# Kernel tuning notes

Hardware: AMD Instinct MI355X
Metric: run time of the kernel (lower is better)

## Reference

```python
import jax, jax.numpy as jnp
import numpy as np

E = 256        # HP.EMBED_SIZE
R = 8          # number of derivation rules / MLPs
S = 512        # number of sequential derivation steps
N = 256        # nodes produced per step
N_INIT = 1024  # initial axiom (thax) embeddings
TOTAL = N_INIT + S * N  # 132096 rows in the vectors buffer
M = 65536      # masked nodes fed to eval_net


def setup_inputs() -> dict:
    key = jax.random.key(0)
    ks = jax.random.split(key, 12)
    rng = np.random.default_rng(0)

    init_vecs = jax.random.normal(ks[0], (N_INIT, E), jnp.float32)
    # rule MLPs: concat(2 parents) -> E (relu) -> E
    W1 = jax.random.normal(ks[1], (R, 2 * E, E), jnp.float32) * (1.0 / np.sqrt(2 * E))
    b1 = jnp.zeros((R, E), jnp.float32)
    W2 = jax.random.normal(ks[2], (R, E, E), jnp.float32) * (1.0 / np.sqrt(E))
    b2 = jnp.zeros((R, E), jnp.float32)
    # eval net: E -> E (relu) -> 1
    eval_W1 = jax.random.normal(ks[3], (E, E), jnp.float32) * (1.0 / np.sqrt(E))
    eval_b1 = jnp.zeros((E,), jnp.float32)
    eval_W2 = jax.random.normal(ks[4], (E, 1), jnp.float32) * (1.0 / np.sqrt(E))
    eval_b2 = jnp.zeros((1,), jnp.float32)

    # step s writes rows [N_INIT + s*N, N_INIT + (s+1)*N)
    ind_steps = (N_INIT + np.arange(S * N, dtype=np.int32)).reshape(S, N)
    # parents drawn causally from already-computed prefix [0, N_INIT + s*N)
    highs = (N_INIT + np.arange(S, dtype=np.int64) * N)[:, None, None]
    pars_ind_steps = (rng.random((S, N, 2)) * highs).astype(np.int32)
    rule_steps = rng.integers(0, R, size=(S,)).astype(np.int32)
    mask = rng.integers(0, TOTAL, size=(M,)).astype(np.int32)

    pos = jax.random.uniform(ks[5], (M,), jnp.float32)
    neg = jax.random.uniform(ks[6], (M,), jnp.float32)
    target = jnp.round(jax.random.uniform(ks[7], (M,), jnp.float32))

    return {
        'init_vecs': init_vecs, 'W1': W1, 'b1': b1, 'W2': W2, 'b2': b2,
        'eval_W1': eval_W1, 'eval_b1': eval_b1, 'eval_W2': eval_W2, 'eval_b2': eval_b2,
        'pos': pos, 'neg': neg, 'target': target,
        'ind_steps': jnp.asarray(ind_steps), 'pars_ind_steps': jnp.asarray(pars_ind_steps),
        'rule_steps': jnp.asarray(rule_steps), 'mask': jnp.asarray(mask),
    }


def reference(init_vecs, W1, b1, W2, b2, eval_W1, eval_b1, eval_W2, eval_b2,
              pos, neg, target, ind_steps, pars_ind_steps, rule_steps, mask):
    vectors = jnp.zeros((TOTAL, E), init_vecs.dtype).at[:N_INIT].set(init_vecs)

    def step(vec, xs):
        inds, pars, r = xs            # [N], [N,2], scalar rule id
        p = vec[pars].reshape(N, 2 * E)   # gather parents
        h = jax.nn.relu(p @ W1[r] + b1[r])
        out = h @ W2[r] + b2[r]
        return vec.at[inds].set(out), None  # scatter new node embeddings

    vectors, _ = jax.lax.scan(step, vectors, (ind_steps, pars_ind_steps, rule_steps))

    x = vectors[mask]
    val = (jax.nn.relu(x @ eval_W1 + eval_b1) @ eval_W2 + eval_b2)[:, 0]

    # pos_weight = POS_WEIGHT_EXTRA * tot_neg / tot_pos (constant w.r.t. grads)
    pw = jax.lax.stop_gradient(jnp.sum(neg) / jnp.maximum(jnp.sum(pos), 1.0))
    # BCEWithLogitsLoss(pos_weight, reduction='none')
    contrib = pw * target * jax.nn.softplus(-val) + (1.0 - target) * jax.nn.softplus(val)
    loss = jnp.sum((pos + neg) * contrib)
    posOK = jnp.sum(pos * (val >= 0))
    negOK = jnp.sum(neg * (val < 0))
    return loss, posOK, negOK
```

## Files before the change

### kernel.cpp

```cpp
#include <hip/hip_runtime.h>
#include <math.h>

#define EMB   256
#define TWOE  512
#define NINIT 1024
#define NSTEP 512
#define NPS   256
#define TOTAL (NINIT + NSTEP * NPS)
#define MM    65536
#define NNODE (NSTEP * NPS)
#define NKEY  2048
#define BTH   512
#define TROWS 32

typedef short s16x8 __attribute__((ext_vector_type(8)));
typedef float f32x4 __attribute__((ext_vector_type(4)));

#define OFF_VECH  0ull
#define OFF_VECL  ((size_t)TOTAL * EMB * 2)
#define OFF_VAL   (2ull * (size_t)TOTAL * EMB * 2)
#define OFF_CNT   (OFF_VAL + (size_t)MM * 4)
#define OFF_ACC   (OFF_CNT + 4096)
#define OFF_PW    (OFF_ACC + 64)
#define OFF_KCNT  (OFF_PW + 192)
#define OFF_KOFS  (OFF_KCNT + (size_t)NKEY * 4)
#define OFF_NL    (OFF_KOFS + (size_t)NKEY * 4)
#define OFF_BROWS (OFF_NL + 256)


__device__ __forceinline__ void store_dev_u32(unsigned* p, unsigned v) {
  asm volatile("global_store_dword %0, %1, off sc0 sc1" :: "v"(p), "v"(v) : "memory");
}
__device__ __forceinline__ void store_dev_b64(void* p, uint2 v) {
  asm volatile("global_store_dwordx2 %0, %1, off sc0 sc1" :: "v"(p), "v"(v) : "memory");
}
__device__ __forceinline__ void store_dev_b128(void* p, uint4 v) {
  store_dev_b64(p, make_uint2(v.x, v.y));
  store_dev_b64((char*)p + 8, make_uint2(v.z, v.w));
}
__device__ __forceinline__ unsigned load_dev_u32(const unsigned* p) {
  unsigned r;
  asm volatile("global_load_dword %0, %1, off sc0 sc1\n\ts_waitcnt vmcnt(0)"
               : "=v"(r) : "v"(p) : "memory");
  return r;
}

__device__ __forceinline__ void gbar_full(unsigned* gc, unsigned* gep) {
  asm volatile("s_waitcnt vmcnt(0)" ::: "memory");
  __syncthreads();
  if (threadIdx.x == 0) {
    unsigned old = __hip_atomic_fetch_add(gc, 1u, __ATOMIC_RELAXED, __HIP_MEMORY_SCOPE_AGENT);
    unsigned tgt = old / 256u + 1u;
    if ((old & 255u) == 255u) store_dev_u32(gep, tgt);
    else while (load_dev_u32(gep) < tgt) __builtin_amdgcn_s_sleep(1);
  }
  __syncthreads();
}

__device__ __forceinline__ void split8(const float* f, uint4& h4, uint4& l4) {
  unsigned hu[8], lu[8];
  #pragma unroll
  for (int i = 0; i < 8; ++i) {
    unsigned u = __builtin_bit_cast(unsigned, f[i]);
    float rh = __builtin_bit_cast(float, u & 0xffff0000u);
    float rl = f[i] - rh;
    hu[i] = u >> 16;
    lu[i] = __builtin_bit_cast(unsigned, rl) >> 16;
  }
  h4 = make_uint4(hu[0] | (hu[1] << 16), hu[2] | (hu[3] << 16),
                  hu[4] | (hu[5] << 16), hu[6] | (hu[7] << 16));
  l4 = make_uint4(lu[0] | (lu[1] << 16), lu[2] | (lu[3] << 16),
                  lu[4] | (lu[5] << 16), lu[6] | (lu[7] << 16));
}

__global__ void zero_scratch(unsigned* cnt, double* acc) {
  for (int i = threadIdx.x; i < 1024; i += 256) cnt[i] = 0u;
  if (threadIdx.x < 8) acc[threadIdx.x] = 0.0;
}

__global__ void init_convert(const float* __restrict__ src,
                             unsigned short* __restrict__ vh,
                             unsigned short* __restrict__ vl) {
  int slot = blockIdx.x * blockDim.x + threadIdx.x;
  float f[8];
  *(float4*)&f[0] = reinterpret_cast<const float4*>(src)[slot * 2];
  *(float4*)&f[4] = reinterpret_cast<const float4*>(src)[slot * 2 + 1];
  uint4 h4, l4;
  split8(f, h4, l4);
  *(uint4*)(vh + (size_t)slot * 8) = h4;
  *(uint4*)(vl + (size_t)slot * 8) = l4;
}

__global__ __launch_bounds__(1024)
void prepass(const int* __restrict__ pars, const int* __restrict__ rules,
             int* __restrict__ kcnt, int* __restrict__ kofs,
             int* __restrict__ brows, int* __restrict__ nlp)
{
  __shared__ unsigned char slvl[TOTAL];
  __shared__ int scnt[NKEY];
  __shared__ int sofs[NKEY];
  __shared__ int swmax[16];
  const int t = threadIdx.x;
  for (int i = t; i < NINIT; i += 1024) slvl[i] = 0;
  for (int k = t; k < NKEY; k += 1024) scnt[k] = 0;
  __syncthreads();
  int lmax = 0;
  for (int s = 0; s < NSTEP; ++s) {
    if (t < NPS) {
      int i = s * NPS + t;
      int l1 = slvl[pars[2 * i]];
      int l2 = slvl[pars[2 * i + 1]];
      int lv = 1 + (l1 > l2 ? l1 : l2);
      slvl[NINIT + i] = (unsigned char)lv;
      if (lv > lmax) lmax = lv;
    }
    __syncthreads();
  }
  for (int o = 32; o; o >>= 1) lmax = max(lmax, __shfl_down(lmax, o));
  if ((t & 63) == 0) swmax[t >> 6] = lmax;
  __syncthreads();
  if (t == 0) {
    int m = 0;
    for (int w = 0; w < 16; ++w) m = max(m, swmax[w]);
    nlp[0] = m;
  }
  for (int i = t; i < NNODE; i += 1024) {
    int key = (int)slvl[NINIT + i] * 8 + rules[i >> 8];
    atomicAdd(&scnt[key], 1);
  }
  __syncthreads();
  if (t == 0) {
    int run = 0;
    for (int k = 0; k < NKEY; ++k) {
      kofs[k] = run; sofs[k] = run; kcnt[k] = scnt[k]; run += scnt[k];
    }
  }
  __syncthreads();
  for (int i = t; i < NNODE; i += 1024) {
    int key = (int)slvl[NINIT + i] * 8 + rules[i >> 8];
    int pos = atomicAdd(&sofs[key], 1);
    brows[pos] = i;
  }
}

__global__ __launch_bounds__(BTH, 1)
void scan_kernel(const float* __restrict__ W1, const float* __restrict__ b1,
                 const float* __restrict__ W2, const float* __restrict__ b2,
                 const int* __restrict__ pars,
                 unsigned short* __restrict__ vech, unsigned short* __restrict__ vecl,
                 const int* __restrict__ kcnt, const int* __restrict__ kofs,
                 const int* __restrict__ brows, const int* __restrict__ nlp,
                 unsigned* __restrict__ cnt)
{
  __shared__ short sW[2][2][8192];
  __shared__ float hL[TROWS][260];
  __shared__ int spar[2 * TROWS];
  __shared__ int sorow[TROWS];
  const int tid = threadIdx.x;
  const int bid = blockIdx.x;
  const int lane = tid & 63;
  const int w = tid >> 6;
  const int rw = w & 1, cw = w >> 1;
  const int row16 = lane & 15, kb8 = (lane >> 4) << 3;
  const int arow = (rw << 4) + row16;
  unsigned* gc  = cnt;
  unsigned* gep = cnt + 32;
  const int NL = nlp[0];
  const int xcd = bid & 7, jb = bid >> 3;

  const int g0 = tid >> 6, l0 = tid & 63;
  const int g1 = g0 + 8,   l1 = l0;

  for (int lv = 1; lv <= NL; ++lv) {
    int cum[9]; cum[0] = 0;
    int cnts[8], ofss[8];
    #pragma unroll
    for (int r = 0; r < 8; ++r) {
      int c = kcnt[lv * 8 + r];
      cnts[r] = c; ofss[r] = kofs[lv * 8 + r];
      cum[r + 1] = cum[r] + ((c + TROWS - 1) >> 5);
    }
    const int G = cum[8];
    const int q = G >> 3, rm = G & 7;
    const int Gx = q + (xcd < rm ? 1 : 0);
    const int sx = xcd * q + (xcd < rm ? xcd : rm);
    for (int j = jb; j < Gx; j += 32) {
      const int g = sx + j;
      int rr = 0;
      while (g >= cum[rr + 1]) ++rr;
      const int t0 = g - cum[rr];
      const int cnt_b = cnts[rr], ofs_b = ofss[rr];
      const int tbase = t0 * TROWS;
      const float* __restrict__ W1r = W1 + (size_t)rr * TWOE * EMB;
      const float* __restrict__ W2r = W2 + (size_t)rr * EMB * EMB;

      __syncthreads();
      if (tid < 2 * TROWS) {
        int slot = tbase + (tid >> 1);
        if (slot >= cnt_b) slot = cnt_b - 1;
        int node = brows[ofs_b + slot];
        spar[tid] = pars[2 * node + (tid & 1)];
        if ((tid & 1) == 0) sorow[tid >> 1] = NINIT + node;
      }
      float f[16];
      {
        const float* p0 = W1r + (size_t)((l0 >> 4) << 3) * EMB + (g0 << 4) + (l0 & 15);
        const float* p1 = W1r + (size_t)((l1 >> 4) << 3) * EMB + (g1 << 4) + (l1 & 15);
        #pragma unroll
        for (int i = 0; i < 8; ++i) { f[i] = p0[i * EMB]; f[8 + i] = p1[i * EMB]; }
        uint4 h4, l4;
        split8(f, h4, l4);
        *(uint4*)&sW[0][0][tid * 8] = h4;
        *(uint4*)&sW[0][1][tid * 8] = l4;
        split8(f + 8, h4, l4);
        *(uint4*)&sW[0][0][(tid + 512) * 8] = h4;
        *(uint4*)&sW[0][1][(tid + 512) * 8] = l4;
      }
      __syncthreads();
      const int par0 = spar[2 * arow], par1 = spar[2 * arow + 1];
      float b1v[4];
      #pragma unroll
      for (int g4 = 0; g4 < 4; ++g4)
        b1v[g4] = b1[rr * EMB + (cw << 6) + (g4 << 4) + row16];

      uint4 ahA, alA;
      {
        size_t off = (size_t)par0 * EMB + kb8;
        ahA = *(const uint4*)(vech + off);
        alA = *(const uint4*)(vecl + off);
      }
      f32x4 acc[4] = {{0,0,0,0},{0,0,0,0},{0,0,0,0},{0,0,0,0}};
      int curb = 0;
      for (int c = 0; c < 16; ++c) {
        const float* nsrc = (c < 15) ? W1r : W2r;
        const int nkb = (c < 15) ? (c + 1) * 32 : 0;
        {
          const float* p0 = nsrc + (size_t)(nkb + ((l0 >> 4) << 3)) * EMB + (g0 << 4) + (l0 & 15);
          const float* p1 = nsrc + (size_t)(nkb + ((l1 >> 4) << 3)) * EMB + (g1 << 4) + (l1 & 15);
          #pragma unroll
          for (int i = 0; i < 8; ++i) { f[i] = p0[i * EMB]; f[8 + i] = p1[i * EMB]; }
        }
        uint4 ahB = ahA, alB = alA;
        if (c < 15) {
          int kglob = (c + 1) * 32 + kb8;
          int par = (kglob >> 8) ? par1 : par0;
          size_t off = (size_t)par * EMB + (kglob & 255);
          ahB = *(const uint4*)(vech + off);
          alB = *(const uint4*)(vecl + off);
        }
        {
          s16x8 Ah = __builtin_bit_cast(s16x8, ahA);
          s16x8 Al = __builtin_bit_cast(s16x8, alA);
          const s16x8* bph = (const s16x8*)&sW[curb][0][0];
          const s16x8* bpl = (const s16x8*)&sW[curb][1][0];
          #pragma unroll
          for (int g4 = 0; g4 < 4; ++g4) {
            int gi = ((cw << 2) + g4) * 64 + lane;
            s16x8 Bh = bph[gi], Bl = bpl[gi];
            acc[g4] = __builtin_amdgcn_mfma_f32_16x16x32_bf16(Ah, Bh, acc[g4], 0, 0, 0);
            acc[g4] = __builtin_amdgcn_mfma_f32_16x16x32_bf16(Ah, Bl, acc[g4], 0, 0, 0);
            acc[g4] = __builtin_amdgcn_mfma_f32_16x16x32_bf16(Al, Bh, acc[g4], 0, 0, 0);
          }
        }
        {
          uint4 h4, l4;
          split8(f, h4, l4);
          *(uint4*)&sW[curb ^ 1][0][tid * 8] = h4;
          *(uint4*)&sW[curb ^ 1][1][tid * 8] = l4;
          split8(f + 8, h4, l4);
          *(uint4*)&sW[curb ^ 1][0][(tid + 512) * 8] = h4;
          *(uint4*)&sW[curb ^ 1][1][(tid + 512) * 8] = l4;
        }
        __syncthreads();
        curb ^= 1;
        ahA = ahB; alA = alB;
      }
      #pragma unroll
      for (int g4 = 0; g4 < 4; ++g4) {
        #pragma unroll
        for (int jj = 0; jj < 4; ++jj)
          hL[(rw << 4) + ((lane >> 4) << 2) + jj][(cw << 6) + (g4 << 4) + row16] =
              fmaxf(acc[g4][jj] + b1v[g4], 0.f);
      }
      __syncthreads();
      float b2v[4];
      #pragma unroll
      for (int g4 = 0; g4 < 4; ++g4)
        b2v[g4] = b2[rr * EMB + (cw << 6) + (g4 << 4) + row16];
      f32x4 acc2[4] = {{0,0,0,0},{0,0,0,0},{0,0,0,0},{0,0,0,0}};
      for (int c2 = 0; c2 < 8; ++c2) {
        if (c2 < 7) {
          const int nkb = (c2 + 1) * 32;
          const float* p0 = W2r + (size_t)(nkb + ((l0 >> 4) << 3)) * EMB + (g0 << 4) + (l0 & 15);
          const float* p1 = W2r + (size_t)(nkb + ((l1 >> 4) << 3)) * EMB + (g1 << 4) + (l1 & 15);
          #pragma unroll
          for (int i = 0; i < 8; ++i) { f[i] = p0[i * EMB]; f[8 + i] = p1[i * EMB]; }
        }
        uint4 a2h4, a2l4;
        {
          int kb = c2 * 32 + kb8;
          float af[8];
          *(float4*)&af[0] = *(const float4*)&hL[arow][kb];
          *(float4*)&af[4] = *(const float4*)&hL[arow][kb + 4];
          split8(af, a2h4, a2l4);
        }
        {
          s16x8 Ah = __builtin_bit_cast(s16x8, a2h4);
          s16x8 Al = __builtin_bit_cast(s16x8, a2l4);
          const s16x8* bph = (const s16x8*)&sW[curb][0][0];
          const s16x8* bpl = (const s16x8*)&sW[curb][1][0];
          #pragma unroll
          for (int g4 = 0; g4 < 4; ++g4) {
            int gi = ((cw << 2) + g4) * 64 + lane;
            s16x8 Bh = bph[gi], Bl = bpl[gi];
            acc2[g4] = __builtin_amdgcn_mfma_f32_16x16x32_bf16(Ah, Bh, acc2[g4], 0, 0, 0);
            acc2[g4] = __builtin_amdgcn_mfma_f32_16x16x32_bf16(Ah, Bl, acc2[g4], 0, 0, 0);
            acc2[g4] = __builtin_amdgcn_mfma_f32_16x16x32_bf16(Al, Bh, acc2[g4], 0, 0, 0);
          }
        }
        if (c2 < 7) {
          uint4 h4, l4;
          split8(f, h4, l4);
          *(uint4*)&sW[curb ^ 1][0][tid * 8] = h4;
          *(uint4*)&sW[curb ^ 1][1][tid * 8] = l4;
          split8(f + 8, h4, l4);
          *(uint4*)&sW[curb ^ 1][0][(tid + 512) * 8] = h4;
          *(uint4*)&sW[curb ^ 1][1][(tid + 512) * 8] = l4;
          __syncthreads();
          curb ^= 1;
        }
      }
      __syncthreads();
      #pragma unroll
      for (int g4 = 0; g4 < 4; ++g4) {
        #pragma unroll
        for (int jj = 0; jj < 4; ++jj)
          hL[(rw << 4) + ((lane >> 4) << 2) + jj][(cw << 6) + (g4 << 4) + row16] =
              acc2[g4][jj] + b2v[g4];
      }
      __syncthreads();
      #pragma unroll
      for (int u = 0; u < 2; ++u) {
        int s = tid + u * 512;
        int row = s >> 5, c8 = (s & 31) * 8;
        float of[8];
        *(float4*)&of[0] = *(const float4*)&hL[row][c8];
        *(float4*)&of[4] = *(const float4*)&hL[row][c8 + 4];
        uint4 h4, l4;
        split8(of, h4, l4);
        if (tbase + row < cnt_b) {
          size_t off = (size_t)sorow[row] * EMB + c8;
          store_dev_b128(vech + off, h4);
          store_dev_b128(vecl + off, l4);
        }
      }
    }
    gbar_full(gc, gep);
  }
}

__global__ void reduce_pn(const float* __restrict__ pos, const float* __restrict__ neg,
                          double* acc) {
  double sp = 0.0, sn = 0.0;
  for (int m = blockIdx.x * blockDim.x + threadIdx.x; m < MM; m += gridDim.x * blockDim.x) {
    sp += (double)pos[m]; sn += (double)neg[m];
  }
  for (int o = 32; o; o >>= 1) { sp += __shfl_down(sp, o); sn += __shfl_down(sn, o); }
  __shared__ double rp[4], rn[4];
  int wid = threadIdx.x >> 6, lane = threadIdx.x & 63;
  if (lane == 0) { rp[wid] = sp; rn[wid] = sn; }
  __syncthreads();
  if (threadIdx.x == 0) {
    double tp = 0.0, tn = 0.0;
    for (int w = 0; w < 4; ++w) { tp += rp[w]; tn += rn[w]; }
    atomicAdd(&acc[0], tp); atomicAdd(&acc[1], tn);
  }
}

__global__ void pw_kernel(const double* __restrict__ acc, float* __restrict__ pw) {
  pw[0] = (float)(acc[1] / fmax(acc[0], 1.0));
}

__global__ __launch_bounds__(256)
void eval_kernel(const unsigned short* __restrict__ vh, const unsigned short* __restrict__ vl,
                 const int* __restrict__ mask,
                 const float* __restrict__ eW1, const float* __restrict__ eb1,
                 const float* __restrict__ eW2, const float* __restrict__ eb2,
                 float* __restrict__ val)
{
  __shared__ float xL[64][36];
  __shared__ float wLx[32][260];
  __shared__ int mrow[64];
  const int tid = threadIdx.x;
  const int a = tid >> 4, b = tid & 15;
  const int m0 = blockIdx.x * 64;
  if (tid < 64) mrow[tid] = mask[m0 + tid];
  __syncthreads();

  float acc[4][16];
  #pragma unroll
  for (int i = 0; i < 4; ++i)
    #pragma unroll
    for (int j = 0; j < 16; ++j) acc[i][j] = 0.f;

  for (int c = 0; c < 8; ++c) {
    const int e0 = c * 32;
    for (int idx = tid; idx < 64 * 4; idx += 256) {
      int rr = idx >> 2, u = idx & 3;
      size_t off = (size_t)mrow[rr] * EMB + e0 + u * 8;
      uint4 hv = *(const uint4*)(vh + off);
      uint4 lv = *(const uint4*)(vl + off);
      const unsigned* hu = (const unsigned*)&hv;
      const unsigned* lu = (const unsigned*)&lv;
      float fo[8];
      #pragma unroll
      for (int jj = 0; jj < 4; ++jj) {
        fo[2 * jj] = __builtin_bit_cast(float, (hu[jj] & 0xffffu) << 16) +
                     __builtin_bit_cast(float, (lu[jj] & 0xffffu) << 16);
        fo[2 * jj + 1] = __builtin_bit_cast(float, hu[jj] & 0xffff0000u) +
                         __builtin_bit_cast(float, lu[jj] & 0xffff0000u);
      }
      *(float4*)&xL[rr][u * 8] = *(float4*)&fo[0];
      *(float4*)&xL[rr][u * 8 + 4] = *(float4*)&fo[4];
    }
    for (int idx = tid; idx < 32 * 64; idx += 256) {
      int e = idx >> 6, k4 = idx & 63;
      reinterpret_cast<float4*>(&wLx[e][0])[k4] =
          reinterpret_cast<const float4*>(eW1 + (size_t)(e0 + e) * EMB)[k4];
    }
    __syncthreads();
    #pragma unroll 4
    for (int e = 0; e < 32; ++e) {
      float xs[4];
      #pragma unroll
      for (int rr = 0; rr < 4; ++rr) xs[rr] = xL[a * 4 + rr][e];
      const float4* wr = reinterpret_cast<const float4*>(&wLx[e][0]) + b * 4;
      float wk[16];
      *reinterpret_cast<float4*>(&wk[0])  = wr[0];
      *reinterpret_cast<float4*>(&wk[4])  = wr[1];
      *reinterpret_cast<float4*>(&wk[8])  = wr[2];
      *reinterpret_cast<float4*>(&wk[12]) = wr[3];
      #pragma unroll
      for (int rr = 0; rr < 4; ++rr)
        #pragma unroll
        for (int kk = 0; kk < 16; ++kk)
          acc[rr][kk] = fmaf(xs[rr], wk[kk], acc[rr][kk]);
    }
    __syncthreads();
  }

  float eb2v = eb2[0];
  float pv[4];
  #pragma unroll
  for (int rr = 0; rr < 4; ++rr) {
    float s = 0.f;
    #pragma unroll
    for (int kk = 0; kk < 16; ++kk) {
      float h = acc[rr][kk] + eb1[b * 16 + kk];
      h = fmaxf(h, 0.f);
      s += h * eW2[b * 16 + kk];
    }
    pv[rr] = s;
  }
  #pragma unroll
  for (int m = 1; m < 16; m <<= 1) {
    #pragma unroll
    for (int rr = 0; rr < 4; ++rr) pv[rr] += __shfl_xor(pv[rr], m);
  }
  if (b == 0) {
    #pragma unroll
    for (int rr = 0; rr < 4; ++rr) val[m0 + a * 4 + rr] = pv[rr] + eb2v;
  }
}

__global__ void loss_kernel(const float* __restrict__ val, const float* __restrict__ pos,
                            const float* __restrict__ neg, const float* __restrict__ tgt,
                            const float* __restrict__ pwp, double* acc)
{
  const float pw = pwp[0];
  double l = 0.0, pk = 0.0, nk = 0.0;
  for (int m = blockIdx.x * blockDim.x + threadIdx.x; m < MM; m += gridDim.x * blockDim.x) {
    float v = val[m], p = pos[m], n = neg[m], t = tgt[m];
    float lp = log1pf(expf(-fabsf(v)));
    float spn = fmaxf(-v, 0.f) + lp;
    float spp = fmaxf(v, 0.f) + lp;
    float contrib = pw * t * spn + (1.f - t) * spp;
    l += (double)((p + n) * contrib);
    if (v >= 0.f) pk += (double)p; else nk += (double)n;
  }
  for (int o = 32; o; o >>= 1) {
    l += __shfl_down(l, o); pk += __shfl_down(pk, o); nk += __shfl_down(nk, o);
  }
  __shared__ double s0[4], s1[4], s2[4];
  int wid = threadIdx.x >> 6, lane = threadIdx.x & 63;
  if (lane == 0) { s0[wid] = l; s1[wid] = pk; s2[wid] = nk; }
  __syncthreads();
  if (threadIdx.x == 0) {
    double ta = 0.0, tb = 0.0, tc = 0.0;
    for (int w = 0; w < 4; ++w) { ta += s0[w]; tb += s1[w]; tc += s2[w]; }
    atomicAdd(&acc[2], ta); atomicAdd(&acc[3], tb); atomicAdd(&acc[4], tc);
  }
}

__global__ void writeout(const double* __restrict__ acc, float* __restrict__ out) {
  if (threadIdx.x == 0) {
    out[0] = (float)acc[2];
    out[1] = (float)acc[3];
    out[2] = (float)acc[4];
  }
}

extern "C" void kernel_launch(void* const* d_in, const int* in_sizes, int n_in,
                              void* d_out, int out_size, void* d_ws, size_t ws_size,
                              hipStream_t stream)
{
  (void)in_sizes; (void)n_in; (void)out_size; (void)ws_size;
  const float* init_vecs = (const float*)d_in[0];
  const float* W1  = (const float*)d_in[1];
  const float* b1  = (const float*)d_in[2];
  const float* W2  = (const float*)d_in[3];
  const float* b2  = (const float*)d_in[4];
  const float* eW1 = (const float*)d_in[5];
  const float* eb1 = (const float*)d_in[6];
  const float* eW2 = (const float*)d_in[7];
  const float* eb2 = (const float*)d_in[8];
  const float* pos = (const float*)d_in[9];
  const float* neg = (const float*)d_in[10];
  const float* tgt = (const float*)d_in[11];
  const int* pars  = (const int*)d_in[13];
  const int* rules = (const int*)d_in[14];
  const int* mask  = (const int*)d_in[15];

  char* ws = (char*)d_ws;
  unsigned short* vech = (unsigned short*)(ws + OFF_VECH);
  unsigned short* vecl = (unsigned short*)(ws + OFF_VECL);
  float*    val   = (float*)(ws + OFF_VAL);
  unsigned* cnt   = (unsigned*)(ws + OFF_CNT);
  double*   acc   = (double*)(ws + OFF_ACC);
  float*    pw    = (float*)(ws + OFF_PW);
  int*      kcnt  = (int*)(ws + OFF_KCNT);
  int*      kofs  = (int*)(ws + OFF_KOFS);
  int*      nlp   = (int*)(ws + OFF_NL);
  int*      brows = (int*)(ws + OFF_BROWS);

  zero_scratch<<<1, 256, 0, stream>>>(cnt, acc);
  prepass<<<1, 1024, 0, stream>>>(pars, rules, kcnt, kofs, brows, nlp);
  init_convert<<<128, 256, 0, stream>>>(init_vecs, vech, vecl);
  scan_kernel<<<256, BTH, 0, stream>>>(W1, b1, W2, b2, pars, vech, vecl,
                                       kcnt, kofs, brows, nlp, cnt);
  reduce_pn<<<128, 256, 0, stream>>>(pos, neg, acc);
  pw_kernel<<<1, 1, 0, stream>>>(acc, pw);
  eval_kernel<<<1024, 256, 0, stream>>>(vech, vecl, mask, eW1, eb1, eW2, eb2, val);
  loss_kernel<<<128, 256, 0, stream>>>(val, pos, neg, tgt, pw, acc);
  writeout<<<1, 1, 0, stream>>>(acc, (float*)d_out);
}
```

Baseline: 1.253 ms.

## Presplit rule weights to bf16 hi/lo once and read MFMA operands from global

Adds a presplit kernel that converts W1/W2 for every rule into a bf16 hi/lo MFMA-ready layout in workspace once per call. The scan kernel then loads B operands straight from global/L2 instead of converting fp32 weights per tile into double-buffered LDS, which removes per-chunk split work and many __syncthreads. The level prepass is also split into its own 256-thread kernel that prefetches parent indices in batches of eight steps, followed by a separate bucketing kernel. The trade-off is that weight reads now depend on L2/global latency with no LDS staging, adding pressure on the memory hierarchy.

```diff
diff --git a/kernel.cpp b/kernel.cpp
--- a/kernel.cpp
+++ b/kernel.cpp
@@ -12,20 +12,24 @@
 #define NKEY  2048
 #define BTH   512
 #define TROWS 32
+#define CHK_SH  16384
+#define RULE_SH (24 * CHK_SH)
 
 typedef short s16x8 __attribute__((ext_vector_type(8)));
 typedef float f32x4 __attribute__((ext_vector_type(4)));
 
-#define OFF_VECH  0ull
-#define OFF_VECL  ((size_t)TOTAL * EMB * 2)
-#define OFF_VAL   (2ull * (size_t)TOTAL * EMB * 2)
-#define OFF_CNT   (OFF_VAL + (size_t)MM * 4)
-#define OFF_ACC   (OFF_CNT + 4096)
-#define OFF_PW    (OFF_ACC + 64)
-#define OFF_KCNT  (OFF_PW + 192)
-#define OFF_KOFS  (OFF_KCNT + (size_t)NKEY * 4)
-#define OFF_NL    (OFF_KOFS + (size_t)NKEY * 4)
-#define OFF_BROWS (OFF_NL + 256)
+#define OFF_VECH   0ull
+#define OFF_VECL   ((size_t)TOTAL * EMB * 2)
+#define OFF_VAL    (2ull * (size_t)TOTAL * EMB * 2)
+#define OFF_CNT    (OFF_VAL + (size_t)MM * 4)
+#define OFF_ACC    (OFF_CNT + 4096)
+#define OFF_PW     (OFF_ACC + 64)
+#define OFF_KCNT   (OFF_PW + 192)
+#define OFF_KOFS   (OFF_KCNT + (size_t)NKEY * 4)
+#define OFF_NL     (OFF_KOFS + (size_t)NKEY * 4)
+#define OFF_BROWS  (OFF_NL + 256)
+#define OFF_LVL8   (OFF_BROWS + (size_t)NNODE * 4)
+#define OFF_WSPLIT (OFF_LVL8 + 132352)
 
 
 __device__ __forceinline__ void store_dev_u32(unsigned* p, unsigned v) {
@@ -91,68 +95,121 @@
   *(uint4*)(vl + (size_t)slot * 8) = l4;
 }
 
+__global__ __launch_bounds__(512)
+void presplit(const float* __restrict__ W1, const float* __restrict__ W2,
+              short* __restrict__ Ws)
+{
+  const int blk = blockIdx.x;
+  const int r = blk / 24, c = blk % 24;
+  const float* src; int kbase;
+  if (c < 16) { src = W1 + (size_t)r * TWOE * EMB; kbase = c * 32; }
+  else        { src = W2 + (size_t)r * EMB * EMB;  kbase = (c - 16) * 32; }
+  short* dst = Ws + (size_t)blk * CHK_SH;
+  const int tid = threadIdx.x;
+  #pragma unroll
+  for (int u = 0; u < 2; ++u) {
+    int qq = tid + u * 512;
+    int g = qq >> 6, l = qq & 63;
+    const float* p = src + (size_t)(kbase + ((l >> 4) << 3)) * EMB + (g << 4) + (l & 15);
+    float f[8];
+    #pragma unroll
+    for (int i = 0; i < 8; ++i) f[i] = p[i * EMB];
+    uint4 h4, l4;
+    split8(f, h4, l4);
+    *(uint4*)(dst + (size_t)qq * 8) = h4;
+    *(uint4*)(dst + 8192 + (size_t)qq * 8) = l4;
+  }
+}
+
+__global__ __launch_bounds__(256)
+void prepass_levels(const int* __restrict__ pars, unsigned char* __restrict__ lvl8,
+                    int* __restrict__ nlp)
+{
+  __shared__ unsigned char slvl[TOTAL];
+  __shared__ int swmax[4];
+  const int t = threadIdx.x;
+  for (int i = t; i < NINIT; i += 256) slvl[i] = 0;
+  __syncthreads();
+  int Pa[8], Pb[8];
+  #pragma unroll
+  for (int w = 0; w < 8; ++w) {
+    Pa[w] = pars[2 * (w * NPS + t)];
+    Pb[w] = pars[2 * (w * NPS + t) + 1];
+  }
+  int lmax = 0;
+  for (int s0 = 0; s0 < NSTEP; s0 += 8) {
+    int Na[8], Nb[8];
+    if (s0 + 8 < NSTEP) {
+      #pragma unroll
+      for (int w = 0; w < 8; ++w) {
+        Na[w] = pars[2 * ((s0 + 8 + w) * NPS + t)];
+        Nb[w] = pars[2 * ((s0 + 8 + w) * NPS + t) + 1];
+      }
+    } else {
+      #pragma unroll
+      for (int w = 0; w < 8; ++w) { Na[w] = 0; Nb[w] = 0; }
+    }
+    #pragma unroll
+    for (int w = 0; w < 8; ++w) {
+      int l1 = slvl[Pa[w]], l2 = slvl[Pb[w]];
+      int lv = 1 + (l1 > l2 ? l1 : l2);
+      slvl[NINIT + (s0 + w) * NPS + t] = (unsigned char)lv;
+      if (lv > lmax) lmax = lv;
+      __syncthreads();
+    }
+    #pragma unroll
+    for (int w = 0; w < 8; ++w) { Pa[w] = Na[w]; Pb[w] = Nb[w]; }
+  }
+  const unsigned* sv = (const unsigned*)slvl;
+  unsigned* gv = (unsigned*)lvl8;
+  for (int i = t; i < TOTAL / 4; i += 256) gv[i] = sv[i];
+  for (int o = 32; o; o >>= 1) lmax = max(lmax, __shfl_down(lmax, o));
+  if ((t & 63) == 0) swmax[t >> 6] = lmax;
+  __syncthreads();
+  if (t == 0) {
+    int m = 0;
+    for (int w = 0; w < 4; ++w) m = max(m, swmax[w]);
+    nlp[0] = m;
+  }
+}
+
 __global__ __launch_bounds__(1024)
-void prepass(const int* __restrict__ pars, const int* __restrict__ rules,
-             int* __restrict__ kcnt, int* __restrict__ kofs,
-             int* __restrict__ brows, int* __restrict__ nlp)
-{
-  __shared__ unsigned char slvl[TOTAL];
+void prepass_bucket(const unsigned char* __restrict__ lvl8, const int* __restrict__ rules,
+                    int* __restrict__ kcnt, int* __restrict__ kofs,
+                    int* __restrict__ brows)
+{
   __shared__ int scnt[NKEY];
   __shared__ int sofs[NKEY];
-  __shared__ int swmax[16];
   const int t = threadIdx.x;
-  for (int i = t; i < NINIT; i += 1024) slvl[i] = 0;
   for (int k = t; k < NKEY; k += 1024) scnt[k] = 0;
   __syncthreads();
-  int lmax = 0;
-  for (int s = 0; s < NSTEP; ++s) {
-    if (t < NPS) {
-      int i = s * NPS + t;
-      int l1 = slvl[pars[2 * i]];
-      int l2 = slvl[pars[2 * i + 1]];
-      int lv = 1 + (l1 > l2 ? l1 : l2);
-      slvl[NINIT + i] = (unsigned char)lv;
-      if (lv > lmax) lmax = lv;
-    }
-    __syncthreads();
-  }
-  for (int o = 32; o; o >>= 1) lmax = max(lmax, __shfl_down(lmax, o));
-  if ((t & 63) == 0) swmax[t >> 6] = lmax;
-  __syncthreads();
-  if (t == 0) {
-    int m = 0;
-    for (int w = 0; w < 16; ++w) m = max(m, swmax[w]);
-    nlp[0] = m;
-  }
   for (int i = t; i < NNODE; i += 1024) {
-    int key = (int)slvl[NINIT + i] * 8 + rules[i >> 8];
+    int key = (int)lvl8[NINIT + i] * 8 + rules[i >> 8];
     atomicAdd(&scnt[key], 1);
   }
   __syncthreads();
   if (t == 0) {
     int run = 0;
     for (int k = 0; k < NKEY; ++k) {
-      kofs[k] = run; sofs[k] = run; kcnt[k] = scnt[k]; run += scnt[k];
+      sofs[k] = run; kofs[k] = run; kcnt[k] = scnt[k]; run += scnt[k];
     }
   }
   __syncthreads();
   for (int i = t; i < NNODE; i += 1024) {
-    int key = (int)slvl[NINIT + i] * 8 + rules[i >> 8];
+    int key = (int)lvl8[NINIT + i] * 8 + rules[i >> 8];
     int pos = atomicAdd(&sofs[key], 1);
     brows[pos] = i;
   }
 }
 
 __global__ __launch_bounds__(BTH, 1)
-void scan_kernel(const float* __restrict__ W1, const float* __restrict__ b1,
-                 const float* __restrict__ W2, const float* __restrict__ b2,
-                 const int* __restrict__ pars,
+void scan_kernel(const short* __restrict__ Ws, const float* __restrict__ b1,
+                 const float* __restrict__ b2, const int* __restrict__ pars,
                  unsigned short* __restrict__ vech, unsigned short* __restrict__ vecl,
                  const int* __restrict__ kcnt, const int* __restrict__ kofs,
                  const int* __restrict__ brows, const int* __restrict__ nlp,
                  unsigned* __restrict__ cnt)
 {
-  __shared__ short sW[2][2][8192];
   __shared__ float hL[TROWS][260];
   __shared__ int spar[2 * TROWS];
   __shared__ int sorow[TROWS];
@@ -160,16 +217,13 @@
   const int bid = blockIdx.x;
   const int lane = tid & 63;
   const int w = tid >> 6;
-  const int rw = w & 1, cw = w >> 1;
+  const int rw = w & 1, cwb = (w >> 1) << 2;
   const int row16 = lane & 15, kb8 = (lane >> 4) << 3;
   const int arow = (rw << 4) + row16;
   unsigned* gc  = cnt;
   unsigned* gep = cnt + 32;
   const int NL = nlp[0];
   const int xcd = bid & 7, jb = bid >> 3;
-
-  const int g0 = tid >> 6, l0 = tid & 63;
-  const int g1 = g0 + 8,   l1 = l0;
 
   for (int lv = 1; lv <= NL; ++lv) {
     int cum[9]; cum[0] = 0;
@@ -191,8 +245,7 @@
       const int t0 = g - cum[rr];
       const int cnt_b = cnts[rr], ofs_b = ofss[rr];
       const int tbase = t0 * TROWS;
-      const float* __restrict__ W1r = W1 + (size_t)rr * TWOE * EMB;
-      const float* __restrict__ W2r = W2 + (size_t)rr * EMB * EMB;
+      const short* __restrict__ Wr = Ws + (size_t)rr * RULE_SH;
 
       __syncthreads();
       if (tid < 2 * TROWS) {
@@ -202,26 +255,12 @@
         spar[tid] = pars[2 * node + (tid & 1)];
         if ((tid & 1) == 0) sorow[tid >> 1] = NINIT + node;
       }
-      float f[16];
-      {
-        const float* p0 = W1r + (size_t)((l0 >> 4) << 3) * EMB + (g0 << 4) + (l0 & 15);
-        const float* p1 = W1r + (size_t)((l1 >> 4) << 3) * EMB + (g1 << 4) + (l1 & 15);
-        #pragma unroll
-        for (int i = 0; i < 8; ++i) { f[i] = p0[i * EMB]; f[8 + i] = p1[i * EMB]; }
-        uint4 h4, l4;
-        split8(f, h4, l4);
-        *(uint4*)&sW[0][0][tid * 8] = h4;
-        *(uint4*)&sW[0][1][tid * 8] = l4;
-        split8(f + 8, h4, l4);
-        *(uint4*)&sW[0][0][(tid + 512) * 8] = h4;
-        *(uint4*)&sW[0][1][(tid + 512) * 8] = l4;
-      }
       __syncthreads();
       const int par0 = spar[2 * arow], par1 = spar[2 * arow + 1];
       float b1v[4];
       #pragma unroll
       for (int g4 = 0; g4 < 4; ++g4)
-        b1v[g4] = b1[rr * EMB + (cw << 6) + (g4 << 4) + row16];
+        b1v[g4] = b1[rr * EMB + ((cwb + g4) << 4) + row16];
 
       uint4 ahA, alA;
       {
@@ -230,16 +269,8 @@
         alA = *(const uint4*)(vecl + off);
       }
       f32x4 acc[4] = {{0,0,0,0},{0,0,0,0},{0,0,0,0},{0,0,0,0}};
-      int curb = 0;
+      #pragma unroll 2
       for (int c = 0; c < 16; ++c) {
-        const float* nsrc = (c < 15) ? W1r : W2r;
-        const int nkb = (c < 15) ? (c + 1) * 32 : 0;
-        {
-          const float* p0 = nsrc + (size_t)(nkb + ((l0 >> 4) << 3)) * EMB + (g0 << 4) + (l0 & 15);
-          const float* p1 = nsrc + (size_t)(nkb + ((l1 >> 4) << 3)) * EMB + (g1 << 4) + (l1 & 15);
-          #pragma unroll
-          for (int i = 0; i < 8; ++i) { f[i] = p0[i * EMB]; f[8 + i] = p1[i * EMB]; }
-        }
         uint4 ahB = ahA, alB = alA;
         if (c < 15) {
           int kglob = (c + 1) * 32 + kb8;
@@ -248,86 +279,52 @@
           ahB = *(const uint4*)(vech + off);
           alB = *(const uint4*)(vecl + off);
         }
-        {
-          s16x8 Ah = __builtin_bit_cast(s16x8, ahA);
-          s16x8 Al = __builtin_bit_cast(s16x8, alA);
-          const s16x8* bph = (const s16x8*)&sW[curb][0][0];
-          const s16x8* bpl = (const s16x8*)&sW[curb][1][0];
-          #pragma unroll
-          for (int g4 = 0; g4 < 4; ++g4) {
-            int gi = ((cw << 2) + g4) * 64 + lane;
-            s16x8 Bh = bph[gi], Bl = bpl[gi];
-            acc[g4] = __builtin_amdgcn_mfma_f32_16x16x32_bf16(Ah, Bh, acc[g4], 0, 0, 0);
-            acc[g4] = __builtin_amdgcn_mfma_f32_16x16x32_bf16(Ah, Bl, acc[g4], 0, 0, 0);
-            acc[g4] = __builtin_amdgcn_mfma_f32_16x16x32_bf16(Al, Bh, acc[g4], 0, 0, 0);
-          }
+        const short* ch = Wr + (size_t)c * CHK_SH;
+        s16x8 Ah = __builtin_bit_cast(s16x8, ahA);
+        s16x8 Al = __builtin_bit_cast(s16x8, alA);
+        #pragma unroll
+        for (int g4 = 0; g4 < 4; ++g4) {
+          int gi = (cwb + g4) * 64 + lane;
+          s16x8 Bh = *(const s16x8*)(ch + (size_t)gi * 8);
+          s16x8 Bl = *(const s16x8*)(ch + 8192 + (size_t)gi * 8);
+          acc[g4] = __builtin_amdgcn_mfma_f32_16x16x32_bf16(Ah, Bh, acc[g4], 0, 0, 0);
+          acc[g4] = __builtin_amdgcn_mfma_f32_16x16x32_bf16(Ah, Bl, acc[g4], 0, 0, 0);
+          acc[g4] = __builtin_amdgcn_mfma_f32_16x16x32_bf16(Al, Bh, acc[g4], 0, 0, 0);
         }
-        {
-          uint4 h4, l4;
-          split8(f, h4, l4);
-          *(uint4*)&sW[curb ^ 1][0][tid * 8] = h4;
-          *(uint4*)&sW[curb ^ 1][1][tid * 8] = l4;
-          split8(f + 8, h4, l4);
-          *(uint4*)&sW[curb ^ 1][0][(tid + 512) * 8] = h4;
-          *(uint4*)&sW[curb ^ 1][1][(tid + 512) * 8] = l4;
-        }
-        __syncthreads();
-        curb ^= 1;
         ahA = ahB; alA = alB;
       }
       #pragma unroll
       for (int g4 = 0; g4 < 4; ++g4) {
         #pragma unroll
         for (int jj = 0; jj < 4; ++jj)
-          hL[(rw << 4) + ((lane >> 4) << 2) + jj][(cw << 6) + (g4 << 4) + row16] =
+          hL[(rw << 4) + ((lane >> 4) << 2) + jj][((cwb + g4) << 4) + row16] =
               fmaxf(acc[g4][jj] + b1v[g4], 0.f);
       }
       __syncthreads();
       float b2v[4];
       #pragma unroll
       for (int g4 = 0; g4 < 4; ++g4)
-        b2v[g4] = b2[rr * EMB + (cw << 6) + (g4 << 4) + row16];
+        b2v[g4] = b2[rr * EMB + ((cwb + g4) << 4) + row16];
       f32x4 acc2[4] = {{0,0,0,0},{0,0,0,0},{0,0,0,0},{0,0,0,0}};
       for (int c2 = 0; c2 < 8; ++c2) {
-        if (c2 < 7) {
-          const int nkb = (c2 + 1) * 32;
-          const float* p0 = W2r + (size_t)(nkb + ((l0 >> 4) << 3)) * EMB + (g0 << 4) + (l0 & 15);
-          const float* p1 = W2r + (size_t)(nkb + ((l1 >> 4) << 3)) * EMB + (g1 << 4) + (l1 & 15);
-          #pragma unroll
-          for (int i = 0; i < 8; ++i) { f[i] = p0[i * EMB]; f[8 + i] = p1[i * EMB]; }
+        const short* ch = Wr + (size_t)(16 + c2) * CHK_SH;
+        uint4 a2h, a2l;
+        {
+          float af[8];
+          *(float4*)&af[0] = *(const float4*)&hL[arow][c2 * 32 + kb8];
+          *(float4*)&af[4] = *(const float4*)&hL[arow][c2 * 32 + kb8 + 4];
+          split8(af, a2h, a2l);
         }
-        uint4 a2h4, a2l4;
-        {
-          int kb = c2 * 32 + kb8;
-          float af[8];
-          *(float4*)&af[0] = *(const float4*)&hL[arow][kb];
-          *(float4*)&af[4] = *(const float4*)&hL[arow][kb + 4];
-          split8(af, a2h4, a2l4);
-        }
-        {
-          s16x8 Ah = __builtin_bit_cast(s16x8, a2h4);
-          s16x8 Al = __builtin_bit_cast(s16x8, a2l4);
-          const s16x8* bph = (const s16x8*)&sW[curb][0][0];
-          const s16x8* bpl = (const s16x8*)&sW[curb][1][0];
-          #pragma unroll
-          for (int g4 = 0; g4 < 4; ++g4) {
-            int gi = ((cw << 2) + g4) * 64 + lane;
-            s16x8 Bh = bph[gi], Bl = bpl[gi];
-            acc2[g4] = __builtin_amdgcn_mfma_f32_16x16x32_bf16(Ah, Bh, acc2[g4], 0, 0, 0);
-            acc2[g4] = __builtin_amdgcn_mfma_f32_16x16x32_bf16(Ah, Bl, acc2[g4], 0, 0, 0);
-            acc2[g4] = __builtin_amdgcn_mfma_f32_16x16x32_bf16(Al, Bh, acc2[g4], 0, 0, 0);
-          }
-        }
-        if (c2 < 7) {
-          uint4 h4, l4;
-          split8(f, h4, l4);
-          *(uint4*)&sW[curb ^ 1][0][tid * 8] = h4;
-          *(uint4*)&sW[curb ^ 1][1][tid * 8] = l4;
-          split8(f + 8, h4, l4);
-          *(uint4*)&sW[curb ^ 1][0][(tid + 512) * 8] = h4;
-          *(uint4*)&sW[curb ^ 1][1][(tid + 512) * 8] = l4;
-          __syncthreads();
-          curb ^= 1;
+        s16x8 Ah = __builtin_bit_cast(s16x8, a2h);
+        s16x8 Al = __builtin_bit_cast(s16x8, a2l);
+        #pragma unroll
+        for (int g4 = 0; g4 < 4; ++g4) {
+          int gi = (cwb + g4) * 64 + lane;
+          s16x8 Bh = *(const s16x8*)(ch + (size_t)gi * 8);
+          s16x8 Bl = *(const s16x8*)(ch + 8192 + (size_t)gi * 8);
+          acc2[g4] = __builtin_amdgcn_mfma_f32_16x16x32_bf16(Ah, Bh, acc2[g4], 0, 0, 0);
+          acc2[g4] = __builtin_amdgcn_mfma_f32_16x16x32_bf16(Ah, Bl, acc2[g4], 0, 0, 0);
+          acc2[g4] = __builtin_amdgcn_mfma_f32_16x16x32_bf16(Al, Bh, acc2[g4], 0, 0, 0);
         }
       }
       __syncthreads();
@@ -335,7 +332,7 @@
       for (int g4 = 0; g4 < 4; ++g4) {
         #pragma unroll
         for (int jj = 0; jj < 4; ++jj)
-          hL[(rw << 4) + ((lane >> 4) << 2) + jj][(cw << 6) + (g4 << 4) + row16] =
+          hL[(rw << 4) + ((lane >> 4) << 2) + jj][((cwb + g4) << 4) + row16] =
               acc2[g4][jj] + b2v[g4];
       }
       __syncthreads();
@@ -542,11 +539,15 @@
   int*      kofs  = (int*)(ws + OFF_KOFS);
   int*      nlp   = (int*)(ws + OFF_NL);
   int*      brows = (int*)(ws + OFF_BROWS);
+  unsigned char* lvl8 = (unsigned char*)(ws + OFF_LVL8);
+  short*    Ws    = (short*)(ws + OFF_WSPLIT);
 
   zero_scratch<<<1, 256, 0, stream>>>(cnt, acc);
-  prepass<<<1, 1024, 0, stream>>>(pars, rules, kcnt, kofs, brows, nlp);
+  prepass_levels<<<1, 256, 0, stream>>>(pars, lvl8, nlp);
+  prepass_bucket<<<1, 1024, 0, stream>>>(lvl8, rules, kcnt, kofs, brows);
   init_convert<<<128, 256, 0, stream>>>(init_vecs, vech, vecl);
-  scan_kernel<<<256, BTH, 0, stream>>>(W1, b1, W2, b2, pars, vech, vecl,
+  presplit<<<192, 512, 0, stream>>>(W1, W2, Ws);
+  scan_kernel<<<256, BTH, 0, stream>>>(Ws, b1, b2, pars, vech, vecl,
                                        kcnt, kofs, brows, nlp, cnt);
   reduce_pn<<<128, 256, 0, stream>>>(pos, neg, acc);
   pw_kernel<<<1, 1, 0, stream>>>(acc, pw);
```

Result: slower. 1.323 ms (+5.6%).
